# Kernel optimization log

Hardware: AMD Instinct MI355X
Metric: run time of the kernel (lower is better)

## Reference

```python
import jax, jax.numpy as jnp
import numpy as np

N, E, D = 20000, 160000, 128   # nodes, edges, d_model
GH, HC = 4, 128                # TransformerConv heads, per-head channels (= out_channels)
MH = 4                         # temporal MHA heads
MC = D // MH                   # temporal MHA per-head dim
EPS = 1e-5


def layer_norm(x, g, b):
    mu = x.mean(-1, keepdims=True)
    var = ((x - mu) ** 2).mean(-1, keepdims=True)
    return (x - mu) * jax.lax.rsqrt(var + EPS) * g + b


def forward(x, temporal_encoding, gq_w, gq_b, gk_w, gk_b, gv_w, gv_b, gs_w, gs_b,
            mha_wq, mha_bq, mha_wk, mha_bk, mha_wv, mha_bv, mha_wo, mha_bo,
            ffn_w1, ffn_b1, ffn_w2, ffn_b2,
            ln1_g, ln1_b, ln2_g, ln2_b, ln3_g, ln3_b, edge_index):
    src, dst = edge_index[0], edge_index[1]
    n = x.shape[0]
    # --- TransformerConv(in=D, out=D, heads=GH, concat=False, root_weight=True) ---
    q = (x @ gq_w.T + gq_b).reshape(n, GH, HC)
    k = (x @ gk_w.T + gk_b).reshape(n, GH, HC)
    v = (x @ gv_w.T + gv_b).reshape(n, GH, HC)
    # per-edge attention logits: <q_i, k_j> / sqrt(out_channels), message j->i
    alpha = (q[dst] * k[src]).sum(-1) / jnp.sqrt(jnp.asarray(HC, x.dtype))  # [E, GH]
    # numerically-stable segment softmax over incoming edges of each dst node
    m = jax.ops.segment_max(alpha, dst, num_segments=n)                     # [N, GH]
    ex = jnp.exp(alpha - m[dst])
    den = jax.ops.segment_sum(ex, dst, num_segments=n)
    w = ex / den[dst]                                                       # [E, GH]
    agg = jax.ops.segment_sum(w[..., None] * v[src], dst, num_segments=n)  # [N, GH, HC]
    graph_out = agg.mean(1) + (x @ gs_w.T + gs_b)  # concat=False -> head mean; + root skip lin
    x1 = layer_norm(x + graph_out, ln1_g, ln1_b)   # dropout is identity at eval
    # --- temporal MHA: per-node query (len 1) attends to its temporal encoding (kv len 1) ---
    tq = (x1 @ mha_wq.T + mha_bq).reshape(n, MH, MC)
    tk = (temporal_encoding @ mha_wk.T + mha_bk).reshape(n, MH, MC)
    tv = (temporal_encoding @ mha_wv.T + mha_bv).reshape(n, MH, MC)
    scores = (tq * tk).sum(-1, keepdims=True) / jnp.sqrt(jnp.asarray(MC, x.dtype))  # [N, MH, 1]
    attn = jax.nn.softmax(scores, axis=-1)  # exactly ones (single kv position); kept for fidelity
    temp_out = (attn * tv).reshape(n, D) @ mha_wo.T + mha_bo
    x2 = layer_norm(x1 + temp_out, ln2_g, ln2_b)
    # --- FFN ---
    h = jax.nn.relu(x2 @ ffn_w1.T + ffn_b1)
    ffn_out = h @ ffn_w2.T + ffn_b2
    return layer_norm(x2 + ffn_out, ln3_g, ln3_b)


def setup_inputs() -> dict:
    ks = jax.random.split(jax.random.key(0), 16)
    s = 0.05
    def p(i, shape):
        return jax.random.normal(ks[i], shape, jnp.float32) * s
    z = lambda *sh: jnp.zeros(sh, jnp.float32)
    o = lambda *sh: jnp.ones(sh, jnp.float32)
    return {
        "x": p(0, (N, D)),
        "temporal_encoding": p(1, (N, D)),
        "gq_w": p(2, (GH * HC, D)), "gq_b": z(GH * HC),
        "gk_w": p(3, (GH * HC, D)), "gk_b": z(GH * HC),
        "gv_w": p(4, (GH * HC, D)), "gv_b": z(GH * HC),
        "gs_w": p(5, (D, D)), "gs_b": z(D),
        "mha_wq": p(6, (D, D)), "mha_bq": z(D),
        "mha_wk": p(7, (D, D)), "mha_bk": z(D),
        "mha_wv": p(8, (D, D)), "mha_bv": z(D),
        "mha_wo": p(9, (D, D)), "mha_bo": z(D),
        "ffn_w1": p(10, (4 * D, D)), "ffn_b1": z(4 * D),
        "ffn_w2": p(11, (D, 4 * D)), "ffn_b2": z(D),
        "ln1_g": o(D), "ln1_b": z(D),
        "ln2_g": o(D), "ln2_b": z(D),
        "ln3_g": o(D), "ln3_b": z(D),
        "edge_index": jax.random.randint(ks[12], (2, E), 0, N, jnp.int32),
    }


def reference(x, temporal_encoding, gq_w, gq_b, gk_w, gk_b, gv_w, gv_b, gs_w, gs_b,
              mha_wq, mha_bq, mha_wk, mha_bk, mha_wv, mha_bv, mha_wo, mha_bo,
              ffn_w1, ffn_b1, ffn_w2, ffn_b2,
              ln1_g, ln1_b, ln2_g, ln2_b, ln3_g, ln3_b, edge_index):
    return forward(x, temporal_encoding, gq_w, gq_b, gk_w, gk_b, gv_w, gv_b, gs_w, gs_b,
                   mha_wq, mha_bq, mha_wk, mha_bk, mha_wv, mha_bv, mha_wo, mha_bo,
                   ffn_w1, ffn_b1, ffn_w2, ffn_b2,
                   ln1_g, ln1_b, ln2_g, ln2_b, ln3_g, ln3_b, edge_index)
```

## Files before the change

### kernel.cpp

```cpp
#include <hip/hip_runtime.h>

#define NN 20000
#define EE 160000
#define DD 128
#define GHC 512
#define INV_SQRT_HC 0.08838834764831845f

typedef __attribute__((ext_vector_type(8))) short short8;
typedef __attribute__((ext_vector_type(4))) short short4v;
typedef __attribute__((ext_vector_type(4))) float float4v;
typedef __attribute__((ext_vector_type(2))) float float2v;
typedef __attribute__((ext_vector_type(4))) unsigned uint4v;
typedef __attribute__((ext_vector_type(2))) unsigned uint2v;

__device__ inline float bf2f(unsigned short u) {
    union { unsigned u; float f; } x; x.u = ((unsigned)u) << 16; return x.f;
}
__device__ inline unsigned short f2bf(float f) {
    union { float f; unsigned u; } x; x.f = f;
    unsigned u = x.u;
    unsigned r = (u + 0x7fffu + ((u >> 16) & 1u)) >> 16;
    return (unsigned short)r;
}
__device__ inline unsigned cvt_pk_bf16(float a, float b) {
    unsigned d;
    asm("v_cvt_pk_bf16_f32 %0, %1, %2" : "=v"(d) : "v"(a), "v"(b));
    return d;
}

__device__ inline void stage16(const short8* gsrc, short8* ldst) {
    __builtin_amdgcn_global_load_lds(
        (const __attribute__((address_space(1))) void*)gsrc,
        (__attribute__((address_space(3))) void*)ldst, 16, 0, 0);
}

#if defined(__has_builtin)
#if __has_builtin(__builtin_amdgcn_cvt_pk_f32_fp8) && __has_builtin(__builtin_amdgcn_cvt_pk_fp8_f32)
#define HW_FP8 1
#endif
#endif
#ifndef HW_FP8
#define HW_FP8 0
#endif

#if !HW_FP8
__device__ inline unsigned char sw_enc_fp8(float f) {
    if (!(f == f)) return 0x7f;
    unsigned s = (f < 0.f) ? 0x80u : 0u;
    float a = fabsf(f);
    if (a >= 448.f) return (unsigned char)(s | 0x7e);
    if (a < 5.96046448e-8f) return (unsigned char)s;
    int e; frexpf(a, &e);
    int E = e - 1;
    if (E < -6) E = -6;
    float q = ldexpf(rintf(ldexpf(a, 3 - E)), E - 3);
    if (q == 0.f) return (unsigned char)s;
    union { float f; unsigned u; } x; x.f = q;
    int qe = (int)((x.u >> 23) & 0xff) - 127;
    if (qe < -6) {
        unsigned mant = (unsigned)rintf(ldexpf(q, 9));
        return (unsigned char)(s | mant);
    }
    unsigned mant = (x.u >> 20) & 7;
    int ebits = qe + 7;
    if (ebits > 15) { ebits = 15; mant = 6; }
    return (unsigned char)(s | ((unsigned)ebits << 3) | mant);
}
__device__ inline float sw_dec_fp8(unsigned char u) {
    unsigned s = u >> 7, e = (u >> 3) & 15, m = u & 7;
    float v = e ? ldexpf((float)(8 + m), (int)e - 10) : ldexpf((float)m, -9);
    return s ? -v : v;
}
#endif

__device__ inline unsigned fp8_enc4(float a, float b, float c, float d) {
#if HW_FP8
    int r = __builtin_amdgcn_cvt_pk_fp8_f32(a, b, 0, false);
    r = __builtin_amdgcn_cvt_pk_fp8_f32(c, d, r, true);
    return (unsigned)r;
#else
    return (unsigned)sw_enc_fp8(a) | ((unsigned)sw_enc_fp8(b) << 8)
         | ((unsigned)sw_enc_fp8(c) << 16) | ((unsigned)sw_enc_fp8(d) << 24);
#endif
}
__device__ inline float2v fp8_dec2_lo(unsigned w) {
#if HW_FP8
    return __builtin_amdgcn_cvt_pk_f32_fp8((int)w, false);
#else
    float2v r;
    r[0] = sw_dec_fp8((unsigned char)(w & 0xff));
    r[1] = sw_dec_fp8((unsigned char)((w >> 8) & 0xff));
    return r;
#endif
}
__device__ inline float2v fp8_dec2_hi(unsigned w) {
#if HW_FP8
    return __builtin_amdgcn_cvt_pk_f32_fp8((int)w, true);
#else
    float2v r;
    r[0] = sw_dec_fp8((unsigned char)((w >> 16) & 0xff));
    r[1] = sw_dec_fp8((unsigned char)(w >> 24));
    return r;
#endif
}

struct WPack { const void* in[18]; };
__device__ __constant__ const int WSZ[18] = {
    65536, 65536, 65536, 512, 512, 512,
    16384, 128, 65536, 512, 65536, 128,
    128, 128, 128, 128, 128, 128 };

__global__ void prep_kernel(const float* __restrict__ x, const float* __restrict__ te,
                            unsigned short* __restrict__ xcout, WPack p,
                            unsigned short* __restrict__ wcout,
                            const float* __restrict__ wv, const float* __restrict__ bv,
                            const float* __restrict__ wo, const float* __restrict__ bo,
                            unsigned short* __restrict__ wcomb,
                            unsigned short* __restrict__ bcomb,
                            const int* __restrict__ e_dst, int* __restrict__ counts)
{
    const int b = blockIdx.x;
    const int tid = threadIdx.x;
    if (b < 1024) {
        const long n4half = (long)NN * DD / 4;
        short4v* out4 = reinterpret_cast<short4v*>(xcout);
        long i = (long)b * 256 + tid;
        const long stride = 1024L * 256;
        const long tot = 2 * n4half;
        for (; i < tot; i += stride) {
            const float4v* src = (i < n4half)
                ? reinterpret_cast<const float4v*>(x)
                : reinterpret_cast<const float4v*>(te) - n4half;
            float4v v = src[i];
            short4v o;
            o[0] = (short)f2bf(v[0]); o[1] = (short)f2bf(v[1]);
            o[2] = (short)f2bf(v[2]); o[3] = (short)f2bf(v[3]);
            out4[i] = o;
        }
    } else if (b < 1600) {
        const int seg = (b - 1024) >> 5;
        const int rep = (b - 1024) & 31;
        int off = 0;
#pragma unroll
        for (int s = 0; s < 18; ++s) if (s < seg) off += WSZ[s];
        const int n = WSZ[seg];
        const float* q = (const float*)p.in[seg];
        for (int i = rep * 256 + tid; i < n; i += 32 * 256)
            wcout[off + i] = f2bf(q[i]);
    } else if (b < 1664) {
        int e = (b - 1600) * 256 + tid;
        int i = e >> 7, kk = e & 127;
        float s = 0.f;
        for (int j = 0; j < 128; ++j)
            s += wo[i * 128 + j] * wv[j * 128 + kk];
        wcomb[e] = f2bf(s);
        if (b == 1600 && tid < 128) {
            float t = 0.f;
            for (int j = 0; j < 128; ++j) t += wo[tid * 128 + j] * bv[j];
            bcomb[tid] = f2bf(t + bo[tid]);
        }
    } else {
        int e = (b - 1664) * 256 + tid;
        if (e < EE) {
            int d = e_dst[e];
            if (d >= 0 && d < NN) atomicAdd(&counts[d], 1);
        }
    }
}

__global__ __launch_bounds__(256) void gemm3_kernel(
    const unsigned short* __restrict__ A, const unsigned short* __restrict__ W,
    const unsigned short* __restrict__ bias, unsigned short* __restrict__ out,
    unsigned char* __restrict__ kvout, int M, int Nout, int split, int relu,
    int nxg, int ncol)
{
    __shared__ short8 wslab[2048];
    __shared__ __attribute__((aligned(16))) unsigned stile4[4][16][32];
    const int tid  = threadIdx.x;
    const int lane = tid & 63;
    const int wid  = tid >> 6;
    const int quad = lane >> 4;
    const int l15  = lane & 15;

    const int nb  = nxg * ncol;
    const int qq  = nb >> 3, rm = nb & 7;
    const int xcd = blockIdx.x & 7, slot = blockIdx.x >> 3;
    const int c   = (xcd < rm) ? xcd * (qq + 1) + slot
                               : rm * (qq + 1) + (xcd - rm) * qq + slot;
    const int xg = c / ncol;
    const int yg = c - xg * ncol;
    const int colbase0 = yg * 128;
    const int rowg = xg * 256;

    const bool isfp8 = (colbase0 >= split);
    const int kvcol = colbase0 - split;
    const int which = isfp8 ? (kvcol >> 9) : 0;
    const int head  = isfp8 ? ((kvcol & 511) >> 7) : 0;

    const short8* A8 = reinterpret_cast<const short8*>(A);
    const short8* W8 = reinterpret_cast<const short8*>(W);

    short8 a4[4];
    {
        int arow = rowg + wid * 16 + l15;
        if (arow >= M) arow = M - 1;
#pragma unroll
        for (int i = 0; i < 4; ++i) a4[i] = A8[(size_t)arow * 16 + i * 4 + quad];
    }

#pragma unroll
    for (int rep = 0; rep < 8; ++rep) {
        const int fi  = (rep * 4 + wid) & 3;
        const int ft  = rep & 3;
        const int ftt = rep >> 2;
        const int wrow = colbase0 + ftt * 64 + 16 * ft + l15;
        stage16(&W8[(size_t)wrow * 16 + fi * 4 + quad], &wslab[rep * 256 + wid * 64]);
    }

    short4v bs4[2][4];
#pragma unroll
    for (int tt = 0; tt < 2; ++tt)
#pragma unroll
        for (int t = 0; t < 4; ++t)
            bs4[tt][t] = *reinterpret_cast<const short4v*>(
                &bias[colbase0 + tt * 64 + 16 * t + quad * 4]);

    __syncthreads();

    unsigned* fpd = &stile4[wid][0][0];

#pragma unroll
    for (int tg = 0; tg < 4; ++tg) {
        const int rowbase = rowg + tg * 64 + wid * 16;

        short8 a4n[4];
        if (tg < 3) {
            int arow = rowbase + 64 + l15;
            if (arow >= M) arow = M - 1;
#pragma unroll
            for (int i = 0; i < 4; ++i) a4n[i] = A8[(size_t)arow * 16 + i * 4 + quad];
        }

#pragma unroll
        for (int tt = 0; tt < 2; ++tt) {
            float4v acc[4];
#pragma unroll
            for (int t = 0; t < 4; ++t) acc[t] = (float4v){0.f, 0.f, 0.f, 0.f};

#pragma unroll
            for (int i = 0; i < 4; ++i) {
#pragma unroll
                for (int t = 0; t < 4; ++t) {
                    short8 wb = wslab[((tt * 4 + t) * 4 + i) * 64 + lane];
                    acc[t] = __builtin_amdgcn_mfma_f32_16x16x32_bf16(wb, a4[i], acc[t], 0, 0, 0);
                }
            }

            if (!isfp8) {
#pragma unroll
                for (int t = 0; t < 4; ++t) {
                    float v0 = acc[t][0] + bf2f((unsigned short)bs4[tt][t][0]);
                    float v1 = acc[t][1] + bf2f((unsigned short)bs4[tt][t][1]);
                    float v2 = acc[t][2] + bf2f((unsigned short)bs4[tt][t][2]);
                    float v3 = acc[t][3] + bf2f((unsigned short)bs4[tt][t][3]);
                    if (relu) {
                        v0 = fmaxf(v0, 0.f); v1 = fmaxf(v1, 0.f);
                        v2 = fmaxf(v2, 0.f); v3 = fmaxf(v3, 0.f);
                    }
                    uint2v d = { cvt_pk_bf16(v0, v1), cvt_pk_bf16(v2, v3) };
                    const int dc = (8 * t + quad * 2) ^ ((l15 & 7) << 2);
                    *reinterpret_cast<uint2v*>(&stile4[wid][l15][dc]) = d;
                }
                const int rr0 = lane >> 3;
                const int cd  = (lane & 7) * 4;
#pragma unroll
                for (int it = 0; it < 2; ++it) {
                    int rw = rr0 + it * 8;
                    int grow = rowbase + rw;
                    if (grow < M) {
                        const int cs = cd ^ ((rw & 7) << 2);
                        uint4v v = *reinterpret_cast<const uint4v*>(&stile4[wid][rw][cs]);
                        *reinterpret_cast<uint4v*>(&out[(size_t)grow * Nout + colbase0 + tt * 64 + cd * 2]) = v;
                    }
                }
            } else {
#pragma unroll
                for (int t = 0; t < 4; ++t) {
                    float v0 = (acc[t][0] + bf2f((unsigned short)bs4[tt][t][0])) * 256.f;
                    float v1 = (acc[t][1] + bf2f((unsigned short)bs4[tt][t][1])) * 256.f;
                    float v2 = (acc[t][2] + bf2f((unsigned short)bs4[tt][t][2])) * 256.f;
                    float v3 = (acc[t][3] + bf2f((unsigned short)bs4[tt][t][3])) * 256.f;
                    const int dc = (tt * 16 + 4 * t + quad) ^ ((l15 & 7) << 2);
                    fpd[l15 * 32 + dc] = fp8_enc4(v0, v1, v2, v3);
                }
            }
        }

        if (isfp8) {
#pragma unroll
            for (int it = 0; it < 2; ++it) {
                int u = lane + it * 64;
                int row = u >> 3;
                int part = u & 7;
                int grow = rowbase + row;
                if (grow < M) {
                    const int db = row * 32 + ((part * 4) ^ ((row & 7) << 2));
                    uint4v v = *reinterpret_cast<const uint4v*>(&fpd[db]);
                    size_t ro = (size_t)grow * 1024 + (size_t)which * 512
                              + (size_t)head * 128 + (size_t)part * 16;
                    *reinterpret_cast<uint4v*>(kvout + ro) = v;
                }
            }
        }

        if (tg < 3) {
#pragma unroll
            for (int i = 0; i < 4; ++i) a4[i] = a4n[i];
        }
    }
}

__global__ __launch_bounds__(256) void gemm_ln2_kernel(
    const unsigned short* __restrict__ A, const unsigned short* __restrict__ W,
    const unsigned short* __restrict__ bias,
    const float* __restrict__ residf, const float* __restrict__ c,
    const unsigned short* __restrict__ g, const unsigned short* __restrict__ beta,
    float* __restrict__ outf, unsigned short* __restrict__ outb, int M, int K)
{
    __shared__ short8 wslab[2048];
    const int tid  = threadIdx.x;
    const int lane = tid & 63;
    const int wid  = tid >> 6;
    const int quad = lane >> 4;
    const int l15  = lane & 15;
    const int rowbase = blockIdx.x * 64 + wid * 16;

    const int grow = rowbase + l15;
    const int gr = (grow < M) ? grow : M - 1;

    const short8* A8 = reinterpret_cast<const short8*>(A);
    const short8* W8 = reinterpret_cast<const short8*>(W);
    const int k8 = K >> 3;
    const int kchunks = K >> 7;

    float4v acc[2][4];
#pragma unroll
    for (int tt = 0; tt < 2; ++tt)
#pragma unroll
        for (int t = 0; t < 4; ++t) acc[tt][t] = (float4v){0.f, 0.f, 0.f, 0.f};

    for (int cc = 0; cc < kchunks; ++cc) {
        if (cc > 0) __syncthreads();
#pragma unroll
        for (int rep = 0; rep < 8; ++rep) {
            const int fi  = (rep * 4 + wid) & 3;
            const int ft  = rep & 3;
            const int ftt = rep >> 2;
            const int wrow = ftt * 64 + 16 * ft + l15;
            stage16(&W8[(size_t)wrow * k8 + cc * 16 + fi * 4 + quad],
                    &wslab[rep * 256 + wid * 64]);
        }
        short8 a4[4];
#pragma unroll
        for (int i = 0; i < 4; ++i) a4[i] = A8[(size_t)gr * k8 + cc * 16 + i * 4 + quad];
        __syncthreads();
#pragma unroll
        for (int tt = 0; tt < 2; ++tt)
#pragma unroll
            for (int i = 0; i < 4; ++i)
#pragma unroll
                for (int t = 0; t < 4; ++t) {
                    short8 wb = wslab[((tt * 4 + t) * 4 + i) * 64 + lane];
                    acc[tt][t] = __builtin_amdgcn_mfma_f32_16x16x32_bf16(wb, a4[i], acc[tt][t], 0, 0, 0);
                }
    }

    float v[32];
#pragma unroll
    for (int tt = 0; tt < 2; ++tt)
#pragma unroll
        for (int t = 0; t < 4; ++t) {
            const int n0 = tt * 64 + 16 * t + quad * 4;
            short4v bs = *reinterpret_cast<const short4v*>(&bias[n0]);
            float4v rv = *reinterpret_cast<const float4v*>(&residf[(size_t)gr * 128 + n0]);
#pragma unroll
            for (int r = 0; r < 4; ++r)
                v[(tt * 4 + t) * 4 + r] = acc[tt][t][r]
                    + bf2f((unsigned short)bs[r]) + rv[r];
        }
    if (c) {
#pragma unroll
        for (int tt = 0; tt < 2; ++tt)
#pragma unroll
            for (int t = 0; t < 4; ++t) {
                const int n0 = tt * 64 + 16 * t + quad * 4;
                float4v cv = *reinterpret_cast<const float4v*>(&c[(size_t)gr * 128 + n0]);
#pragma unroll
                for (int r = 0; r < 4; ++r) v[(tt * 4 + t) * 4 + r] += cv[r];
            }
    }
    float s = 0.f, sq = 0.f;
#pragma unroll
    for (int i = 0; i < 32; ++i) { s += v[i]; sq += v[i] * v[i]; }
    s  += __shfl_xor(s, 16, 64);  s  += __shfl_xor(s, 32, 64);
    sq += __shfl_xor(sq, 16, 64); sq += __shfl_xor(sq, 32, 64);
    float mu  = s * (1.f / 128.f);
    float var = sq * (1.f / 128.f) - mu * mu;
    float rs  = rsqrtf(fmaxf(var, 0.f) + 1e-5f);

    if (grow < M) {
#pragma unroll
        for (int tt = 0; tt < 2; ++tt)
#pragma unroll
            for (int t = 0; t < 4; ++t) {
                const int n0 = tt * 64 + 16 * t + quad * 4;
                short4v gg = *reinterpret_cast<const short4v*>(&g[n0]);
                short4v bb = *reinterpret_cast<const short4v*>(&beta[n0]);
                float4v ov;
#pragma unroll
                for (int r = 0; r < 4; ++r)
                    ov[r] = (v[(tt * 4 + t) * 4 + r] - mu) * rs
                            * bf2f((unsigned short)gg[r]) + bf2f((unsigned short)bb[r]);
                *reinterpret_cast<float4v*>(&outf[(size_t)grow * 128 + n0]) = ov;
                if (outb) {
                    uint2v d = { cvt_pk_bf16(ov[0], ov[1]), cvt_pk_bf16(ov[2], ov[3]) };
                    *reinterpret_cast<uint2v*>(&outb[(size_t)grow * 128 + n0]) = d;
                }
            }
    }
}

__global__ __launch_bounds__(256) void gemm_ln12_kernel(
    const unsigned short* __restrict__ A1, const unsigned short* __restrict__ W1,
    const unsigned short* __restrict__ b1,
    const float* __restrict__ rx, const float* __restrict__ ragg,
    const unsigned short* __restrict__ g1, const unsigned short* __restrict__ be1,
    const unsigned short* __restrict__ A2, const unsigned short* __restrict__ W2,
    const unsigned short* __restrict__ b2,
    const unsigned short* __restrict__ g2, const unsigned short* __restrict__ be2,
    float* __restrict__ outf, unsigned short* __restrict__ outb, int M)
{
    __shared__ short8 wslab[2048];
    const int tid  = threadIdx.x;
    const int lane = tid & 63;
    const int wid  = tid >> 6;
    const int quad = lane >> 4;
    const int l15  = lane & 15;
    const int rowbase = blockIdx.x * 64 + wid * 16;

    const int grow = rowbase + l15;
    const int gr = (grow < M) ? grow : M - 1;

    const short8* A81 = reinterpret_cast<const short8*>(A1);
    const short8* A82 = reinterpret_cast<const short8*>(A2);
    const short8* W81 = reinterpret_cast<const short8*>(W1);
    const short8* W82 = reinterpret_cast<const short8*>(W2);

#pragma unroll
    for (int rep = 0; rep < 8; ++rep) {
        const int fi  = (rep * 4 + wid) & 3;
        const int ft  = rep & 3;
        const int ftt = rep >> 2;
        const int wrow = ftt * 64 + 16 * ft + l15;
        stage16(&W81[(size_t)wrow * 16 + fi * 4 + quad], &wslab[rep * 256 + wid * 64]);
    }
    short8 a4[4];
#pragma unroll
    for (int i = 0; i < 4; ++i) a4[i] = A81[(size_t)gr * 16 + i * 4 + quad];
    __syncthreads();

    float4v acc1[2][4];
#pragma unroll
    for (int tt = 0; tt < 2; ++tt)
#pragma unroll
        for (int t = 0; t < 4; ++t) acc1[tt][t] = (float4v){0.f, 0.f, 0.f, 0.f};
#pragma unroll
    for (int tt = 0; tt < 2; ++tt)
#pragma unroll
        for (int i = 0; i < 4; ++i)
#pragma unroll
            for (int t = 0; t < 4; ++t) {
                short8 wb = wslab[((tt * 4 + t) * 4 + i) * 64 + lane];
                acc1[tt][t] = __builtin_amdgcn_mfma_f32_16x16x32_bf16(wb, a4[i], acc1[tt][t], 0, 0, 0);
            }
    __syncthreads();

#pragma unroll
    for (int rep = 0; rep < 8; ++rep) {
        const int fi  = (rep * 4 + wid) & 3;
        const int ft  = rep & 3;
        const int ftt = rep >> 2;
        const int wrow = ftt * 64 + 16 * ft + l15;
        stage16(&W82[(size_t)wrow * 16 + fi * 4 + quad], &wslab[rep * 256 + wid * 64]);
    }
    short8 a42[4];
#pragma unroll
    for (int i = 0; i < 4; ++i) a42[i] = A82[(size_t)gr * 16 + i * 4 + quad];

    float x1[32];
    {
        float v[32];
#pragma unroll
        for (int tt = 0; tt < 2; ++tt)
#pragma unroll
            for (int t = 0; t < 4; ++t) {
                const int n0 = tt * 64 + 16 * t + quad * 4;
                short4v bs = *reinterpret_cast<const short4v*>(&b1[n0]);
                float4v rv = *reinterpret_cast<const float4v*>(&rx[(size_t)gr * 128 + n0]);
                float4v cv = *reinterpret_cast<const float4v*>(&ragg[(size_t)gr * 128 + n0]);
#pragma unroll
                for (int r = 0; r < 4; ++r)
                    v[(tt * 4 + t) * 4 + r] = acc1[tt][t][r]
                        + bf2f((unsigned short)bs[r]) + rv[r] + cv[r];
            }
        float s = 0.f, sq = 0.f;
#pragma unroll
        for (int i = 0; i < 32; ++i) { s += v[i]; sq += v[i] * v[i]; }
        s  += __shfl_xor(s, 16, 64);  s  += __shfl_xor(s, 32, 64);
        sq += __shfl_xor(sq, 16, 64); sq += __shfl_xor(sq, 32, 64);
        float mu  = s * (1.f / 128.f);
        float var = sq * (1.f / 128.f) - mu * mu;
        float rs  = rsqrtf(fmaxf(var, 0.f) + 1e-5f);
#pragma unroll
        for (int tt = 0; tt < 2; ++tt)
#pragma unroll
            for (int t = 0; t < 4; ++t) {
                const int n0 = tt * 64 + 16 * t + quad * 4;
                short4v gg = *reinterpret_cast<const short4v*>(&g1[n0]);
                short4v bb = *reinterpret_cast<const short4v*>(&be1[n0]);
#pragma unroll
                for (int r = 0; r < 4; ++r)
                    x1[(tt * 4 + t) * 4 + r] = (v[(tt * 4 + t) * 4 + r] - mu) * rs
                        * bf2f((unsigned short)gg[r]) + bf2f((unsigned short)bb[r]);
            }
    }

    __syncthreads();

    float4v acc2[2][4];
#pragma unroll
    for (int tt = 0; tt < 2; ++tt)
#pragma unroll
        for (int t = 0; t < 4; ++t) acc2[tt][t] = (float4v){0.f, 0.f, 0.f, 0.f};
#pragma unroll
    for (int tt = 0; tt < 2; ++tt)
#pragma unroll
        for (int i = 0; i < 4; ++i)
#pragma unroll
            for (int t = 0; t < 4; ++t) {
                short8 wb = wslab[((tt * 4 + t) * 4 + i) * 64 + lane];
                acc2[tt][t] = __builtin_amdgcn_mfma_f32_16x16x32_bf16(wb, a42[i], acc2[tt][t], 0, 0, 0);
            }

    float v[32];
#pragma unroll
    for (int tt = 0; tt < 2; ++tt)
#pragma unroll
        for (int t = 0; t < 4; ++t) {
            const int n0 = tt * 64 + 16 * t + quad * 4;
            short4v bs = *reinterpret_cast<const short4v*>(&b2[n0]);
#pragma unroll
            for (int r = 0; r < 4; ++r)
                v[(tt * 4 + t) * 4 + r] = acc2[tt][t][r]
                    + bf2f((unsigned short)bs[r]) + x1[(tt * 4 + t) * 4 + r];
        }
    float s = 0.f, sq = 0.f;
#pragma unroll
    for (int i = 0; i < 32; ++i) { s += v[i]; sq += v[i] * v[i]; }
    s  += __shfl_xor(s, 16, 64);  s  += __shfl_xor(s, 32, 64);
    sq += __shfl_xor(sq, 16, 64); sq += __shfl_xor(sq, 32, 64);
    float mu  = s * (1.f / 128.f);
    float var = sq * (1.f / 128.f) - mu * mu;
    float rs  = rsqrtf(fmaxf(var, 0.f) + 1e-5f);

    if (grow < M) {
#pragma unroll
        for (int tt = 0; tt < 2; ++tt)
#pragma unroll
            for (int t = 0; t < 4; ++t) {
                const int n0 = tt * 64 + 16 * t + quad * 4;
                short4v gg = *reinterpret_cast<const short4v*>(&g2[n0]);
                short4v bb = *reinterpret_cast<const short4v*>(&be2[n0]);
                float4v ov;
#pragma unroll
                for (int r = 0; r < 4; ++r)
                    ov[r] = (v[(tt * 4 + t) * 4 + r] - mu) * rs
                            * bf2f((unsigned short)gg[r]) + bf2f((unsigned short)bb[r]);
                *reinterpret_cast<float4v*>(&outf[(size_t)grow * 128 + n0]) = ov;
                uint2v d = { cvt_pk_bf16(ov[0], ov[1]), cvt_pk_bf16(ov[2], ov[3]) };
                *reinterpret_cast<uint2v*>(&outb[(size_t)grow * 128 + n0]) = d;
            }
    }
}

__global__ __launch_bounds__(1024) void scan_kernel(
    const int* __restrict__ counts, int* __restrict__ offsets, int* __restrict__ pos, int n)
{
    __shared__ int wsum[16];
    __shared__ int carry_s;
    const int tid = threadIdx.x;
    const int wid = tid >> 6, lane = tid & 63;
    int vals[20];
#pragma unroll
    for (int cI = 0; cI < 20; ++cI) {
        int i = cI * 1024 + tid;
        vals[cI] = (i < n) ? counts[i] : 0;
    }
    if (tid == 0) carry_s = 0;
    __syncthreads();
#pragma unroll
    for (int cI = 0; cI < 20; ++cI) {
        int i = cI * 1024 + tid;
        int val = vals[cI];
        int x = val;
#pragma unroll
        for (int off = 1; off < 64; off <<= 1) {
            int t = __shfl_up(x, off, 64);
            if (lane >= off) x += t;
        }
        if (lane == 63) wsum[wid] = x;
        __syncthreads();
        if (wid == 0 && lane < 16) {
            int s = wsum[lane];
#pragma unroll
            for (int off = 1; off < 16; off <<= 1) {
                int t = __shfl_up(s, off, 64);
                if (lane >= off) s += t;
            }
            wsum[lane] = s;
        }
        __syncthreads();
        int prefix = (wid > 0 ? wsum[wid - 1] : 0) + carry_s;
        int ex = prefix + x - val;
        if (i < n) { offsets[i] = ex; pos[i] = ex; }
        __syncthreads();
        if (tid == 0) carry_s += wsum[15];
        __syncthreads();
    }
    if (tid == 0) offsets[n] = carry_s;
}

__global__ void scatter_kernel(const int* __restrict__ src, const int* __restrict__ dst,
                               int* __restrict__ pos, int* __restrict__ sorted_src, int E)
{
    int e = blockIdx.x * 256 + threadIdx.x;
    if (e < E) {
        int d = dst[e];
        if (d >= 0 && d < NN) {
            int p = atomicAdd(&pos[d], 1);
            if (p >= 0 && p < E) sorted_src[p] = src[e];
        }
    }
}

__device__ inline void agg_edge(const uint2v& kk, const uint2v& vv,
                                const float* qf, float* acc, float& ssum)
{
    float2v k01 = fp8_dec2_lo(kk[0]);
    float2v k23 = fp8_dec2_hi(kk[0]);
    float2v k45 = fp8_dec2_lo(kk[1]);
    float2v k67 = fp8_dec2_hi(kk[1]);
    float dot = qf[0] * k01[0] + qf[1] * k01[1] + qf[2] * k23[0] + qf[3] * k23[1]
              + qf[4] * k45[0] + qf[5] * k45[1] + qf[6] * k67[0] + qf[7] * k67[1];
    dot += __shfl_xor(dot, 1, 64);
    dot += __shfl_xor(dot, 2, 64);
    dot += __shfl_xor(dot, 4, 64);
    dot += __shfl_xor(dot, 8, 64);
    float pp = __expf(dot);
    ssum += pp;
    float2v v01 = fp8_dec2_lo(vv[0]);
    float2v v23 = fp8_dec2_hi(vv[0]);
    float2v v45 = fp8_dec2_lo(vv[1]);
    float2v v67 = fp8_dec2_hi(vv[1]);
    acc[0] += pp * v01[0]; acc[1] += pp * v01[1];
    acc[2] += pp * v23[0]; acc[3] += pp * v23[1];
    acc[4] += pp * v45[0]; acc[5] += pp * v45[1];
    acc[6] += pp * v67[0]; acc[7] += pp * v67[1];
}

__global__ __launch_bounds__(256) void agg_kernel(
    const unsigned short* __restrict__ q, const unsigned char* __restrict__ kvb,
    const int* __restrict__ offsets, const int* __restrict__ srcs,
    float* __restrict__ aggb)
{
    __shared__ float sacc[4][64][8];
    __shared__ float sssum[4][64];
    const int tid  = threadIdx.x;
    const int wid  = tid >> 6;
    const int lane = tid & 63;
    const int node = blockIdx.x * 2 + (wid >> 1);
    const int half = wid & 1;

    const short8* q8 = reinterpret_cast<const short8*>(q);
    const int fidx = (lane >> 4) * 16 + (lane & 15);
    const int koff = fidx * 8;

    short8 qv = q8[(size_t)node * 64 + fidx];
    float qf[8];
#pragma unroll
    for (int i = 0; i < 8; ++i)
        qf[i] = bf2f((unsigned short)qv[i]) * (INV_SQRT_HC / 256.f);

    int beg = offsets[node], end = offsets[node + 1];
    if (beg < 0) beg = 0;
    if (end > EE) end = EE;
    float ssum = 0.f;
    float acc[8];
#pragma unroll
    for (int i = 0; i < 8; ++i) acc[i] = 0.f;

    const int start = beg + half;
    int nce = (end > start) ? ((end - start + 1) >> 1) : 0;
    int ncap = (nce > 64) ? 64 : nce;

    int sv = 0;
    if (lane < ncap) {
        int s = srcs[start + 2 * lane];
        if (s < 0) s = 0;
        if (s >= NN) s = NN - 1;
        sv = s;
    }
    if (ncap > 0) {
        int s0 = __shfl(sv, 0, 64);
        uint2v kc = *reinterpret_cast<const uint2v*>(kvb + (size_t)s0 * 1024 + koff);
        uint2v vc = *reinterpret_cast<const uint2v*>(kvb + (size_t)s0 * 1024 + 512 + koff);
        for (int i = 0; i < ncap; ++i) {
            uint2v kn, vn;
            if (i + 1 < ncap) {
                int sn = __shfl(sv, i + 1, 64);
                kn = *reinterpret_cast<const uint2v*>(kvb + (size_t)sn * 1024 + koff);
                vn = *reinterpret_cast<const uint2v*>(kvb + (size_t)sn * 1024 + 512 + koff);
            }
            agg_edge(kc, vc, qf, acc, ssum);
            kc = kn; vc = vn;
        }
    }
    for (int j = start + 128; j < end; j += 2) {
        int s = srcs[j];
        if (s < 0) s = 0;
        if (s >= NN) s = NN - 1;
        uint2v kc = *reinterpret_cast<const uint2v*>(kvb + (size_t)s * 1024 + koff);
        uint2v vc = *reinterpret_cast<const uint2v*>(kvb + (size_t)s * 1024 + 512 + koff);
        agg_edge(kc, vc, qf, acc, ssum);
    }

#pragma unroll
    for (int i = 0; i < 8; ++i) sacc[wid][lane][i] = acc[i];
    sssum[wid][lane] = ssum;
    __syncthreads();
    if (half == 0) {
#pragma unroll
        for (int i = 0; i < 8; ++i) acc[i] += sacc[wid ^ 1][lane][i];
        ssum += sssum[wid ^ 1][lane];

        float inv = (ssum > 0.f) ? 1.f / (256.f * ssum) : 0.f;
#pragma unroll
        for (int i = 0; i < 8; ++i) acc[i] *= inv;
#pragma unroll
        for (int i = 0; i < 8; ++i) {
            acc[i] += __shfl_xor(acc[i], 16, 64);
            acc[i] += __shfl_xor(acc[i], 32, 64);
            acc[i] *= 0.25f;
        }
        if (lane < 16) {
            float4v* o = reinterpret_cast<float4v*>(aggb + (size_t)node * 128 + lane * 8);
            o[0] = (float4v){acc[0], acc[1], acc[2], acc[3]};
            o[1] = (float4v){acc[4], acc[5], acc[6], acc[7]};
        }
    }
}

extern "C" void kernel_launch(void* const* d_in, const int* in_sizes, int n_in,
                              void* d_out, int out_size, void* d_ws, size_t ws_size,
                              hipStream_t stream)
{
    const int* edge_index = (const int*)d_in[28];
    const int* e_src = edge_index;
    const int* e_dst = edge_index + EE;

    if (n_in < 29 || in_sizes[0] != NN * DD || in_sizes[28] != 2 * EE || out_size != NN * DD)
        return;

    const size_t SZ_OFF  = (size_t)(NN + 16) * 4;
    const size_t SZ_CNT  = (size_t)NN * 4;
    const size_t SZ_SS   = (size_t)EE * 4;
    const size_t SZ_SM   = (size_t)NN * DD * 2;
    const size_t SZ_F32  = (size_t)NN * DD * 4;
    const size_t SZ_Q    = (size_t)NN * 512 * 2;
    const size_t SZ_KV   = (size_t)NN * 1024;
    const size_t SZ_HB   = (size_t)NN * GHC * 2;
    const size_t WC_ELE  = 347136;
    const size_t SZ_WC   = WC_ELE * 2;
    const size_t SZ_WCB  = 16384 * 2 + 256;
    const size_t REQUIRED = SZ_OFF + 2 * SZ_CNT + SZ_SS + 2 * SZ_SM + SZ_WC + SZ_WCB
                          + SZ_Q + SZ_KV + 3 * SZ_F32 + SZ_SM + SZ_HB;

    if (ws_size < REQUIRED) return;

    char* w = (char*)d_ws;
    int* offsets = (int*)w;        w += SZ_OFF;
    int* counts  = (int*)w;        w += SZ_CNT;
    int* pos     = (int*)w;        w += SZ_CNT;
    int* sorted_src = (int*)w;     w += SZ_SS;
    unsigned short* xc   = (unsigned short*)w; w += SZ_SM;
    unsigned short* tec  = (unsigned short*)w; w += SZ_SM;
    unsigned short* wc   = (unsigned short*)w; w += SZ_WC;
    unsigned short* wcomb = (unsigned short*)w; w += 16384 * 2;
    unsigned short* bcomb = (unsigned short*)w; w += 256;
    unsigned short* qb   = (unsigned short*)w; w += SZ_Q;
    unsigned char*  kvb  = (unsigned char*)w;  w += SZ_KV;
    float*          aggb = (float*)w;          w += SZ_F32;
    float*          x1f  = (float*)w;          w += SZ_F32;
    float*          x2f  = (float*)w;          w += SZ_F32;
    unsigned short* x2b  = (unsigned short*)w; w += SZ_SM;
    unsigned short* hbuf = (unsigned short*)w; w += SZ_HB;
    (void)x1f;

    unsigned short* cw = wc;
    unsigned short* qkv_w = cw; cw += 3 * 65536;
    unsigned short* qkv_b = cw; cw += 3 * 512;
    unsigned short* gs_w  = cw; cw += 16384;  unsigned short* gs_b  = cw; cw += 128;
    unsigned short* ffn_w1 = cw; cw += 65536; unsigned short* ffn_b1 = cw; cw += 512;
    unsigned short* ffn_w2 = cw; cw += 65536; unsigned short* ffn_b2 = cw; cw += 128;
    unsigned short* ln1_g = cw; cw += 128;    unsigned short* ln1_b = cw; cw += 128;
    unsigned short* ln2_g = cw; cw += 128;    unsigned short* ln2_b = cw; cw += 128;
    unsigned short* ln3_g = cw; cw += 128;    unsigned short* ln3_b = cw; cw += 128;

    const int EB = (EE + 255) / 256;
    const dim3 blk(256);
    const int MB = (NN + 63) / 64;
    const int MB2 = (NN + 255) / 256;

    WPack pack;
    const int live_idx[18] = {2,4,6, 3,5,7, 8,9, 18,19, 20,21, 22,23,24,25,26,27};
    for (int i = 0; i < 18; ++i) pack.in[i] = d_in[live_idx[i]];

    (void)hipMemsetAsync(counts, 0, SZ_CNT, stream);
    prep_kernel<<<1664 + EB, blk, 0, stream>>>((const float*)d_in[0], (const float*)d_in[1],
                                               xc, pack, wc,
                                               (const float*)d_in[14], (const float*)d_in[15],
                                               (const float*)d_in[16], (const float*)d_in[17],
                                               wcomb, bcomb, e_dst, counts);

    scan_kernel<<<1, 1024, 0, stream>>>(counts, offsets, pos, NN);
    scatter_kernel<<<EB, blk, 0, stream>>>(e_src, e_dst, pos, sorted_src, EE);

    gemm3_kernel<<<dim3(MB2 * 12), blk, 0, stream>>>(xc, qkv_w, qkv_b, qb, kvb,
                                                     NN, 512, 512, 0, MB2, 12);
    agg_kernel<<<NN / 2, blk, 0, stream>>>(qb, kvb, offsets, sorted_src, aggb);
    gemm_ln12_kernel<<<MB, blk, 0, stream>>>(xc, gs_w, gs_b,
                                             (const float*)d_in[0], aggb,
                                             ln1_g, ln1_b,
                                             tec, wcomb, bcomb,
                                             ln2_g, ln2_b, x2f, x2b, NN);
    gemm3_kernel<<<dim3(MB2 * 4), blk, 0, stream>>>(x2b, ffn_w1, ffn_b1, hbuf, nullptr,
                                                    NN, 512, 99999, 1, MB2, 4);
    gemm_ln2_kernel<<<MB, blk, 0, stream>>>(hbuf, ffn_w2, ffn_b2, x2f, nullptr,
                                            ln3_g, ln3_b, (float*)d_out, nullptr, NN, GHC);
}
```

Measured before the change: 258.4 us.

## Fuse FFN up-projection, ReLU and down-projection with LayerNorm into one kernel

Replaces the separate FFN1 GEMM kernel and the FFN2+LayerNorm kernel with one kernel. For each 128-wide chunk of the hidden dimension it computes the up-projection plus bias and ReLU, stores the bf16 result in a swizzled shared-memory tile, and immediately accumulates it into the down-projection. This avoids writing and re-reading the 20000x512 hidden activation buffer in global memory and drops one kernel launch. In exchange each block now stages both weight matrices, adds more barriers per chunk, and uses more LDS, which may reduce occupancy.

```diff
diff --git a/kernel.cpp b/kernel.cpp
--- a/kernel.cpp
+++ b/kernel.cpp
@@ -320,50 +320,101 @@
     }
 }
 
-__global__ __launch_bounds__(256) void gemm_ln2_kernel(
-    const unsigned short* __restrict__ A, const unsigned short* __restrict__ W,
-    const unsigned short* __restrict__ bias,
-    const float* __restrict__ residf, const float* __restrict__ c,
+__global__ __launch_bounds__(256) void gemm_ffn_ln_kernel(
+    const unsigned short* __restrict__ A,
+    const unsigned short* __restrict__ W1,
+    const unsigned short* __restrict__ b1,
+    const unsigned short* __restrict__ W2,
+    const unsigned short* __restrict__ b2,
+    const float* __restrict__ residf,
     const unsigned short* __restrict__ g, const unsigned short* __restrict__ beta,
-    float* __restrict__ outf, unsigned short* __restrict__ outb, int M, int K)
+    float* __restrict__ outf, int M)
 {
     __shared__ short8 wslab[2048];
+    __shared__ __attribute__((aligned(16))) unsigned short htile[64 * 128];
     const int tid  = threadIdx.x;
     const int lane = tid & 63;
     const int wid  = tid >> 6;
     const int quad = lane >> 4;
     const int l15  = lane & 15;
     const int rowbase = blockIdx.x * 64 + wid * 16;
-
     const int grow = rowbase + l15;
     const int gr = (grow < M) ? grow : M - 1;
-
-    const short8* A8 = reinterpret_cast<const short8*>(A);
-    const short8* W8 = reinterpret_cast<const short8*>(W);
-    const int k8 = K >> 3;
-    const int kchunks = K >> 7;
-
-    float4v acc[2][4];
+    const int hrow = wid * 16 + l15;
+    char* hb = reinterpret_cast<char*>(htile);
+
+    const short8* A8  = reinterpret_cast<const short8*>(A);
+    const short8* W18 = reinterpret_cast<const short8*>(W1);
+    const short8* W28 = reinterpret_cast<const short8*>(W2);
+
+    short8 a4[4];
+#pragma unroll
+    for (int i = 0; i < 4; ++i) a4[i] = A8[(size_t)gr * 16 + i * 4 + quad];
+
+    float4v acc2[2][4];
 #pragma unroll
     for (int tt = 0; tt < 2; ++tt)
 #pragma unroll
-        for (int t = 0; t < 4; ++t) acc[tt][t] = (float4v){0.f, 0.f, 0.f, 0.f};
-
-    for (int cc = 0; cc < kchunks; ++cc) {
-        if (cc > 0) __syncthreads();
+        for (int t = 0; t < 4; ++t) acc2[tt][t] = (float4v){0.f, 0.f, 0.f, 0.f};
+
+    for (int cc = 0; cc < 4; ++cc) {
+        __syncthreads();
+#pragma unroll
+        for (int rep = 0; rep < 8; ++rep) {
+            const int fi  = (rep * 4 + wid) & 3;
+            const int ft  = rep & 3;
+            const int ftt = rep >> 2;
+            const int wrow = cc * 128 + ftt * 64 + 16 * ft + l15;
+            stage16(&W18[(size_t)wrow * 16 + fi * 4 + quad], &wslab[rep * 256 + wid * 64]);
+        }
+        __syncthreads();
+
+        float4v acc1[2][4];
+#pragma unroll
+        for (int tt = 0; tt < 2; ++tt)
+#pragma unroll
+            for (int t = 0; t < 4; ++t) acc1[tt][t] = (float4v){0.f, 0.f, 0.f, 0.f};
+#pragma unroll
+        for (int tt = 0; tt < 2; ++tt)
+#pragma unroll
+            for (int i = 0; i < 4; ++i)
+#pragma unroll
+                for (int t = 0; t < 4; ++t) {
+                    short8 wb = wslab[((tt * 4 + t) * 4 + i) * 64 + lane];
+                    acc1[tt][t] = __builtin_amdgcn_mfma_f32_16x16x32_bf16(wb, a4[i], acc1[tt][t], 0, 0, 0);
+                }
+#pragma unroll
+        for (int tt = 0; tt < 2; ++tt)
+#pragma unroll
+            for (int t = 0; t < 4; ++t) {
+                const int n0 = tt * 64 + 16 * t + quad * 4;
+                short4v bs = *reinterpret_cast<const short4v*>(&b1[cc * 128 + n0]);
+                float v0 = fmaxf(acc1[tt][t][0] + bf2f((unsigned short)bs[0]), 0.f);
+                float v1 = fmaxf(acc1[tt][t][1] + bf2f((unsigned short)bs[1]), 0.f);
+                float v2 = fmaxf(acc1[tt][t][2] + bf2f((unsigned short)bs[2]), 0.f);
+                float v3 = fmaxf(acc1[tt][t][3] + bf2f((unsigned short)bs[3]), 0.f);
+                uint2v d = { cvt_pk_bf16(v0, v1), cvt_pk_bf16(v2, v3) };
+                *reinterpret_cast<uint2v*>(
+                    hb + ((hrow * 256 + n0 * 2) ^ ((hrow & 7) << 4))) = d;
+            }
+
+        __syncthreads();
 #pragma unroll
         for (int rep = 0; rep < 8; ++rep) {
             const int fi  = (rep * 4 + wid) & 3;
             const int ft  = rep & 3;
             const int ftt = rep >> 2;
             const int wrow = ftt * 64 + 16 * ft + l15;
-            stage16(&W8[(size_t)wrow * k8 + cc * 16 + fi * 4 + quad],
+            stage16(&W28[(size_t)wrow * 64 + cc * 16 + fi * 4 + quad],
                     &wslab[rep * 256 + wid * 64]);
         }
-        short8 a4[4];
-#pragma unroll
-        for (int i = 0; i < 4; ++i) a4[i] = A8[(size_t)gr * k8 + cc * 16 + i * 4 + quad];
         __syncthreads();
+
+        short8 h4[4];
+#pragma unroll
+        for (int i = 0; i < 4; ++i)
+            h4[i] = *reinterpret_cast<const short8*>(
+                hb + ((hrow * 256 + (i * 32 + quad * 8) * 2) ^ ((hrow & 7) << 4)));
 #pragma unroll
         for (int tt = 0; tt < 2; ++tt)
 #pragma unroll
@@ -371,7 +422,7 @@
 #pragma unroll
                 for (int t = 0; t < 4; ++t) {
                     short8 wb = wslab[((tt * 4 + t) * 4 + i) * 64 + lane];
-                    acc[tt][t] = __builtin_amdgcn_mfma_f32_16x16x32_bf16(wb, a4[i], acc[tt][t], 0, 0, 0);
+                    acc2[tt][t] = __builtin_amdgcn_mfma_f32_16x16x32_bf16(wb, h4[i], acc2[tt][t], 0, 0, 0);
                 }
     }
 
@@ -381,24 +432,13 @@
 #pragma unroll
         for (int t = 0; t < 4; ++t) {
             const int n0 = tt * 64 + 16 * t + quad * 4;
-            short4v bs = *reinterpret_cast<const short4v*>(&bias[n0]);
+            short4v bs = *reinterpret_cast<const short4v*>(&b2[n0]);
             float4v rv = *reinterpret_cast<const float4v*>(&residf[(size_t)gr * 128 + n0]);
 #pragma unroll
             for (int r = 0; r < 4; ++r)
-                v[(tt * 4 + t) * 4 + r] = acc[tt][t][r]
+                v[(tt * 4 + t) * 4 + r] = acc2[tt][t][r]
                     + bf2f((unsigned short)bs[r]) + rv[r];
         }
-    if (c) {
-#pragma unroll
-        for (int tt = 0; tt < 2; ++tt)
-#pragma unroll
-            for (int t = 0; t < 4; ++t) {
-                const int n0 = tt * 64 + 16 * t + quad * 4;
-                float4v cv = *reinterpret_cast<const float4v*>(&c[(size_t)gr * 128 + n0]);
-#pragma unroll
-                for (int r = 0; r < 4; ++r) v[(tt * 4 + t) * 4 + r] += cv[r];
-            }
-    }
     float s = 0.f, sq = 0.f;
 #pragma unroll
     for (int i = 0; i < 32; ++i) { s += v[i]; sq += v[i] * v[i]; }
@@ -422,10 +462,6 @@
                     ov[r] = (v[(tt * 4 + t) * 4 + r] - mu) * rs
                             * bf2f((unsigned short)gg[r]) + bf2f((unsigned short)bb[r]);
                 *reinterpret_cast<float4v*>(&outf[(size_t)grow * 128 + n0]) = ov;
-                if (outb) {
-                    uint2v d = { cvt_pk_bf16(ov[0], ov[1]), cvt_pk_bf16(ov[2], ov[3]) };
-                    *reinterpret_cast<uint2v*>(&outb[(size_t)grow * 128 + n0]) = d;
-                }
             }
     }
 }
@@ -814,7 +850,7 @@
     float*          x2f  = (float*)w;          w += SZ_F32;
     unsigned short* x2b  = (unsigned short*)w; w += SZ_SM;
     unsigned short* hbuf = (unsigned short*)w; w += SZ_HB;
-    (void)x1f;
+    (void)x1f; (void)hbuf;
 
     unsigned short* cw = wc;
     unsigned short* qkv_w = cw; cw += 3 * 65536;
@@ -853,8 +889,6 @@
                                              ln1_g, ln1_b,
                                              tec, wcomb, bcomb,
                                              ln2_g, ln2_b, x2f, x2b, NN);
-    gemm3_kernel<<<dim3(MB2 * 4), blk, 0, stream>>>(x2b, ffn_w1, ffn_b1, hbuf, nullptr,
-                                                    NN, 512, 99999, 1, MB2, 4);
-    gemm_ln2_kernel<<<MB, blk, 0, stream>>>(hbuf, ffn_w2, ffn_b2, x2f, nullptr,
-                                            ln3_g, ln3_b, (float*)d_out, nullptr, NN, GHC);
-}
+    gemm_ffn_ln_kernel<<<MB, blk, 0, stream>>>(x2b, ffn_w1, ffn_b1, ffn_w2, ffn_b2,
+                                               x2f, ln3_g, ln3_b, (float*)d_out, NN);
+}
```

Measured after the change: 262.7 us. No clear change (+1.7%).
